# Optimization experiments

Hardware: AMD Instinct MI355X
Metric: run time of the kernel (lower is better)

Reference implementation:

```python
import jax, jax.numpy as jnp
import numpy as np

K = 7          # kernel_size
GC = 16        # group_channels (hardcoded in module)
EPS = 1e-5     # BatchNorm eps


def setup_inputs() -> dict:
    key = jax.random.key(0)
    ks = jax.random.split(key, 4)
    B, C, H, W = 4, 256, 56, 56
    Cr = C // 4                      # reduction_ratio = 4
    G = C // GC                      # groups = 16
    return {
        "x": jax.random.normal(ks[0], (B, C, H, W), jnp.float32),
        "conv1_w": jax.random.normal(ks[1], (Cr, C), jnp.float32) * 0.05,
        "bn_gamma": jnp.ones((Cr,), jnp.float32),
        "bn_beta": jnp.zeros((Cr,), jnp.float32),
        "bn_mean": jnp.zeros((Cr,), jnp.float32),
        "bn_var": jnp.ones((Cr,), jnp.float32),
        "conv2_w": jax.random.normal(ks[2], (K * K * G, Cr), jnp.float32) * 0.05,
        "conv2_b": jax.random.normal(ks[3], (K * K * G,), jnp.float32) * 0.05,
    }


def _unfold(x, k):
    # torch nn.Unfold with padding=(k-1)//2, stride=1 -> [B, C, k*k, H, W]
    B, C, H, W = x.shape
    p = (k - 1) // 2
    xp = jnp.pad(x, ((0, 0), (0, 0), (p, p), (p, p)))
    patches = jnp.stack(
        [xp[:, :, i:i + H, j:j + W] for i in range(k) for j in range(k)],
        axis=2,
    )  # (kh, kw) flattened, channel-slowest -> matches torch unfold layout
    return patches


def reference(x, conv1_w, bn_gamma, bn_beta, bn_mean, bn_var, conv2_w, conv2_b):
    B, C, H, W = x.shape
    G = C // GC
    # kernel-generation branch (stride == 1, no avgpool)
    w = jnp.einsum('bchw,oc->bohw', x, conv1_w)                 # conv1 1x1
    inv_std = jax.lax.rsqrt(bn_var + EPS)
    w = (w - bn_mean[None, :, None, None]) * (bn_gamma * inv_std)[None, :, None, None] \
        + bn_beta[None, :, None, None]                           # BN (eval)
    w = jax.nn.relu(w)
    w = jnp.einsum('bchw,oc->bohw', w, conv2_w) + conv2_b[None, :, None, None]
    w = w.reshape(B, G, K * K, H, W)                             # [B,G,K2,H,W]
    # unfold + weighted reduce
    patches = _unfold(x, K).reshape(B, G, GC, K * K, H, W)       # [B,G,gc,K2,H,W]
    out = jnp.einsum('bgkhw,bgckhw->bgchw', w, patches)          # sum over K2
    return out.reshape(B, C, H, W)
```

## Files before the change

kernel.cpp:

```cpp
#include <hip/hip_runtime.h>


#define EPS 1e-5f

typedef __fp16 half2t __attribute__((ext_vector_type(2)));
typedef __fp16 half8t __attribute__((ext_vector_type(8)));
typedef float floatx4 __attribute__((ext_vector_type(4)));

__device__ inline half8t pack8(float4 u0, float4 u1, float s) {
    half8t a;
    half2t q;
    q = __builtin_amdgcn_cvt_pkrtz(u0.x * s, u0.y * s); a[0] = q[0]; a[1] = q[1];
    q = __builtin_amdgcn_cvt_pkrtz(u0.z * s, u0.w * s); a[2] = q[0]; a[3] = q[1];
    q = __builtin_amdgcn_cvt_pkrtz(u1.x * s, u1.y * s); a[4] = q[0]; a[5] = q[1];
    q = __builtin_amdgcn_cvt_pkrtz(u1.z * s, u1.w * s); a[6] = q[0]; a[7] = q[1];
    return a;
}

__global__ __launch_bounds__(256, 4) void k1_conv1(
    const float* __restrict__ x, const float* __restrict__ w1,
    const float* __restrict__ gamma, const float* __restrict__ beta,
    const float* __restrict__ mean, const float* __restrict__ var,
    __fp16* __restrict__ mid)
{
    __shared__ __align__(16) __fp16 lxB[32 * 72];
    const int t    = threadIdx.x;
    const int b    = blockIdx.y;
    const int p0   = blockIdx.x * 32;
    const int lane = t & 63, wvid = t >> 6;
    const int mrow = lane & 15, quad = lane >> 4;

    const int orow = wvid * 16 + mrow;
    const float s = gamma[orow] * rsqrtf(var[orow] + EPS);
    half8t A[4][2];
#pragma unroll
    for (int ch = 0; ch < 4; ++ch)
#pragma unroll
        for (int h = 0; h < 2; ++h) {
            const float* src = &w1[orow * 256 + ch * 64 + h * 32 + quad * 8];
            A[ch][h] = pack8(*(const float4*)src, *(const float4*)(src + 4), s);
        }

    floatx4 acc[2] = {};
    const int c2 = t & 31, pxq = t >> 5;
    for (int ch = 0; ch < 4; ++ch) {
        const float* r0 = &x[(size_t)(b * 256 + ch * 64 + 2 * c2) * 3136 + p0 + pxq * 4];
        const float* r1 = r0 + 3136;
        float4 a0 = *(const float4*)r0;
        float4 b0 = *(const float4*)r1;
        const float* f0 = (const float*)&a0;
        const float* f1 = (const float*)&b0;
#pragma unroll
        for (int j = 0; j < 4; ++j) {
            half2t q = __builtin_amdgcn_cvt_pkrtz(f0[j], f1[j]);
            *(half2t*)&lxB[(pxq * 4 + j) * 72 + 2 * c2] = q;
        }
        __syncthreads();
#pragma unroll
        for (int pt = 0; pt < 2; ++pt) {
            half8t bf0 = *(const half8t*)&lxB[(pt * 16 + mrow) * 72 + quad * 8];
            half8t bf1 = *(const half8t*)&lxB[(pt * 16 + mrow) * 72 + quad * 8 + 32];
            acc[pt] = __builtin_amdgcn_mfma_f32_16x16x32_f16(A[ch][0], bf0, acc[pt], 0, 0, 0);
            acc[pt] = __builtin_amdgcn_mfma_f32_16x16x32_f16(A[ch][1], bf1, acc[pt], 0, 0, 0);
        }
        __syncthreads();
    }
    float bb[4];
#pragma unroll
    for (int i = 0; i < 4; ++i) {
        int o = wvid * 16 + quad * 4 + i;
        float so = gamma[o] * rsqrtf(var[o] + EPS);
        bb[i] = beta[o] - mean[o] * so;
    }
#pragma unroll
    for (int pt = 0; pt < 2; ++pt)
#pragma unroll
        for (int i = 0; i < 4; ++i) {
            float v = fmaxf(acc[pt][i] + bb[i], 0.f);
            lxB[(pt * 16 + mrow) * 72 + wvid * 16 + quad * 4 + i] = (__fp16)v;
        }
    __syncthreads();
    {
        int px = t >> 3, o8 = t & 7;
        *(half8t*)&mid[(size_t)(b * 3136 + p0 + px) * 64 + o8 * 8] =
            *(const half8t*)&lxB[px * 72 + o8 * 8];
    }
}

__global__ __launch_bounds__(256, 5) void k23_fused(
    const float* __restrict__ x, const __fp16* __restrict__ mid,
    const float* __restrict__ cw, const float* __restrict__ cb,
    float* __restrict__ out)
{
    __shared__ __align__(16) unsigned char smem[28944];
    __fp16* lmid = (__fp16*)smem;
    float*  lx   = (float*)smem;
    float*  lw2  = (float*)(smem + 15616);

    const int t  = threadIdx.x;
    const int b  = blockIdx.z;
    const int g  = blockIdx.y;
    const int th = blockIdx.x / 7, tw = blockIdx.x % 7;
    const int h0 = th * 8, w0 = tw * 8;
    const int lane = t & 63, wvid = t >> 6;
    const int mrow = lane & 15, quad = lane >> 4;

    float4 rv4[4];
    int    rslot[4];
#pragma unroll
    for (int i = 0; i < 4; ++i) {
        int s = t + i * 256;
        rslot[i] = s;
        float4 v = make_float4(0.f, 0.f, 0.f, 0.f);
        if (s < 896) {
            int ch = s / 56, r = s % 56;
            int row = r >> 2, q = r & 3;
            int gh = h0 + row - 3;
            int gwb = w0 - 4 + q * 4;
            bool ok = (gh >= 0) & (gh < 56) & (gwb >= 0) & (gwb <= 52);
            int ghc = min(max(gh, 0), 55);
            int gwc = min(max(gwb, 0), 52);
            float4 ld = *(const float4*)&x[(size_t)(b * 256 + g * 16 + ch) * 3136 +
                                           ghc * 56 + gwc];
            if (ok) v = ld;
        }
        rv4[i] = v;
    }

    const int krow = wvid * 16 + mrow;
    half8t a0 = {}, a1 = {};
    if (krow < 49) {
        const float* src = &cw[(size_t)(g * 49 + krow) * 64 + quad * 8];
        a0 = pack8(*(const float4*)src,        *(const float4*)(src + 4),  1.f);
        a1 = pack8(*(const float4*)(src + 32), *(const float4*)(src + 36), 1.f);
    }

#pragma unroll
    for (int i = 0; i < 2; ++i) {
        int s  = t + i * 256;
        int px = s >> 3, c8 = s & 7;
        int pix = (h0 + (px >> 3)) * 56 + w0 + (px & 7);
        *(half8t*)&lmid[px * 72 + c8 * 8] =
            *(const half8t*)&mid[(size_t)(b * 3136 + pix) * 64 + c8 * 8];
    }
    __syncthreads();

    {
        float bias[4];
        int   kor[4];
#pragma unroll
        for (int i = 0; i < 4; ++i) {
            kor[i]  = wvid * 16 + quad * 4 + i;
            bias[i] = (kor[i] < 49) ? cb[g * 49 + kor[i]] : 0.f;
        }
#pragma unroll
        for (int pt = 0; pt < 4; ++pt) {
            half8t b0 = *(const half8t*)&lmid[(pt * 16 + mrow) * 72 + quad * 8];
            half8t b1 = *(const half8t*)&lmid[(pt * 16 + mrow) * 72 + quad * 8 + 32];
            floatx4 acc = {0.f, 0.f, 0.f, 0.f};
            acc = __builtin_amdgcn_mfma_f32_16x16x32_f16(a0, b0, acc, 0, 0, 0);
            acc = __builtin_amdgcn_mfma_f32_16x16x32_f16(a1, b1, acc, 0, 0, 0);
#pragma unroll
            for (int i = 0; i < 4; ++i)
                if (kor[i] < 49)
                    lw2[kor[i] * 68 + pt * 16 + mrow] = acc[i] + bias[i];
        }
    }
    __syncthreads();

#pragma unroll
    for (int i = 0; i < 4; ++i) {
        int s = rslot[i];
        if (s < 896) {
            int ch = s / 56, r = s % 56;
            int row = r >> 2, q = r & 3;
            float* dst = &lx[ch * 244 + row * 17 + q * 4];
            dst[0] = rv4[i].x; dst[1] = rv4[i].y;
            dst[2] = rv4[i].z; dst[3] = rv4[i].w;
        }
    }
    __syncthreads();

    const int cc = t >> 4, pxt = t & 15;
    const int sh = pxt >> 1, sw4 = (pxt & 1) * 4;
    float a0f = 0.f, a1f = 0.f, a2f = 0.f, a3f = 0.f;
#pragma unroll
    for (int kh = 0; kh < 7; ++kh) {
        float xr[10];
        const int base = cc * 244 + (sh + kh) * 17 + sw4 + 1;
#pragma unroll
        for (int j = 0; j < 10; ++j) xr[j] = lx[base + j];
#pragma unroll
        for (int kw = 0; kw < 7; ++kw) {
            const float4 wv = *(const float4*)&lw2[(kh * 7 + kw) * 68 + pxt * 4];
            a0f = fmaf(wv.x, xr[kw + 0], a0f);
            a1f = fmaf(wv.y, xr[kw + 1], a1f);
            a2f = fmaf(wv.z, xr[kw + 2], a2f);
            a3f = fmaf(wv.w, xr[kw + 3], a3f);
        }
    }
    *(float4*)&out[(b * 256 + g * 16 + cc) * 3136 + (h0 + sh) * 56 + w0 + sw4] =
        make_float4(a0f, a1f, a2f, a3f);
}

extern "C" void kernel_launch(void* const* d_in, const int* in_sizes, int n_in,
                              void* d_out, int out_size, void* d_ws, size_t ws_size,
                              hipStream_t stream) {
    const float* x     = (const float*)d_in[0];
    const float* w1    = (const float*)d_in[1];
    const float* gamma = (const float*)d_in[2];
    const float* beta  = (const float*)d_in[3];
    const float* mean  = (const float*)d_in[4];
    const float* var   = (const float*)d_in[5];
    const float* cw    = (const float*)d_in[6];
    const float* cb    = (const float*)d_in[7];
    float* out = (float*)d_out;

    __fp16* mid = (__fp16*)d_ws;

    k1_conv1<<<dim3(98, 4), 256, 0, stream>>>(x, w1, gamma, beta, mean, var, mid);
    k23_fused<<<dim3(49, 16, 4), 256, 0, stream>>>(x, mid, cw, cb, out);
}
```

Measured before the change: 106.8 us.

## Process two groups per block with fp16 staging and register-blocked unfold

Restructures the fused kernel so each 128-thread block handles two groups, one wave per group. Each wave computes all 49 dynamic kernel rows for its group with MFMA, reusing the shared mid tile across both groups. The x halo tile and the generated weights are now stored in LDS as fp16 instead of fp32, roughly halving LDS footprint and traffic. The inner unfold loop is register-blocked over 4 channels × 4 pixels so each loaded weight vector is reused across several channels. The risks are extra fp16 rounding in x and the weights, a higher register load (14 half4 prefetch registers plus a 16-float accumulator), and fewer threads per block.

```diff
diff --git a/kernel.cpp b/kernel.cpp
--- a/kernel.cpp
+++ b/kernel.cpp
@@ -4,6 +4,7 @@
 #define EPS 1e-5f
 
 typedef __fp16 half2t __attribute__((ext_vector_type(2)));
+typedef __fp16 half4t __attribute__((ext_vector_type(4)));
 typedef __fp16 half8t __attribute__((ext_vector_type(8)));
 typedef float floatx4 __attribute__((ext_vector_type(4)));
 
@@ -87,57 +88,48 @@
     }
 }
 
-__global__ __launch_bounds__(256, 5) void k23_fused(
+__global__ __launch_bounds__(128, 3) void k2_fused(
     const float* __restrict__ x, const __fp16* __restrict__ mid,
     const float* __restrict__ cw, const float* __restrict__ cb,
     float* __restrict__ out)
 {
-    __shared__ __align__(16) unsigned char smem[28944];
+    __shared__ __align__(16) unsigned char smem[28960];
     __fp16* lmid = (__fp16*)smem;
-    float*  lx   = (float*)smem;
-    float*  lw2  = (float*)(smem + 15616);
+    __fp16* lxh  = (__fp16*)smem;
 
     const int t  = threadIdx.x;
     const int b  = blockIdx.z;
-    const int g  = blockIdx.y;
+    const int gq = blockIdx.y;
     const int th = blockIdx.x / 7, tw = blockIdx.x % 7;
     const int h0 = th * 8, w0 = tw * 8;
     const int lane = t & 63, wvid = t >> 6;
     const int mrow = lane & 15, quad = lane >> 4;
-
-    float4 rv4[4];
-    int    rslot[4];
+    const int g = gq * 2 + wvid;
+    __fp16* lw2h = (__fp16*)(smem + 14848 + wvid * 7056);
+
+    half4t hr[14];
+#pragma unroll
+    for (int i = 0; i < 14; ++i) {
+        int s = t + i * 128;
+        int ch = s / 56, r = s % 56;
+        int row = r >> 2, cq = r & 3;
+        int gh = h0 + row - 3;
+        int gwb = w0 - 4 + cq * 4;
+        bool ok = (gh >= 0) & (gh < 56) & (gwb >= 0) & (gwb <= 52);
+        int ghc = min(max(gh, 0), 55);
+        int gwc = min(max(gwb, 0), 52);
+        float4 ld = *(const float4*)&x[(size_t)(b * 256 + gq * 32 + ch) * 3136 +
+                                       ghc * 56 + gwc];
+        if (!ok) ld = make_float4(0.f, 0.f, 0.f, 0.f);
+        half2t p0 = __builtin_amdgcn_cvt_pkrtz(ld.x, ld.y);
+        half2t p1 = __builtin_amdgcn_cvt_pkrtz(ld.z, ld.w);
+        half4t h; h[0] = p0[0]; h[1] = p0[1]; h[2] = p1[0]; h[3] = p1[1];
+        hr[i] = h;
+    }
+
 #pragma unroll
     for (int i = 0; i < 4; ++i) {
-        int s = t + i * 256;
-        rslot[i] = s;
-        float4 v = make_float4(0.f, 0.f, 0.f, 0.f);
-        if (s < 896) {
-            int ch = s / 56, r = s % 56;
-            int row = r >> 2, q = r & 3;
-            int gh = h0 + row - 3;
-            int gwb = w0 - 4 + q * 4;
-            bool ok = (gh >= 0) & (gh < 56) & (gwb >= 0) & (gwb <= 52);
-            int ghc = min(max(gh, 0), 55);
-            int gwc = min(max(gwb, 0), 52);
-            float4 ld = *(const float4*)&x[(size_t)(b * 256 + g * 16 + ch) * 3136 +
-                                           ghc * 56 + gwc];
-            if (ok) v = ld;
-        }
-        rv4[i] = v;
-    }
-
-    const int krow = wvid * 16 + mrow;
-    half8t a0 = {}, a1 = {};
-    if (krow < 49) {
-        const float* src = &cw[(size_t)(g * 49 + krow) * 64 + quad * 8];
-        a0 = pack8(*(const float4*)src,        *(const float4*)(src + 4),  1.f);
-        a1 = pack8(*(const float4*)(src + 32), *(const float4*)(src + 36), 1.f);
-    }
-
-#pragma unroll
-    for (int i = 0; i < 2; ++i) {
-        int s  = t + i * 256;
+        int s  = t + i * 128;
         int px = s >> 3, c8 = s & 7;
         int pix = (h0 + (px >> 3)) * 56 + w0 + (px & 7);
         *(half8t*)&lmid[px * 72 + c8 * 8] =
@@ -146,61 +138,80 @@
     __syncthreads();
 
     {
-        float bias[4];
-        int   kor[4];
-#pragma unroll
-        for (int i = 0; i < 4; ++i) {
-            kor[i]  = wvid * 16 + quad * 4 + i;
-            bias[i] = (kor[i] < 49) ? cb[g * 49 + kor[i]] : 0.f;
-        }
+        half8t bf[4][2];
 #pragma unroll
         for (int pt = 0; pt < 4; ++pt) {
-            half8t b0 = *(const half8t*)&lmid[(pt * 16 + mrow) * 72 + quad * 8];
-            half8t b1 = *(const half8t*)&lmid[(pt * 16 + mrow) * 72 + quad * 8 + 32];
-            floatx4 acc = {0.f, 0.f, 0.f, 0.f};
-            acc = __builtin_amdgcn_mfma_f32_16x16x32_f16(a0, b0, acc, 0, 0, 0);
-            acc = __builtin_amdgcn_mfma_f32_16x16x32_f16(a1, b1, acc, 0, 0, 0);
-#pragma unroll
-            for (int i = 0; i < 4; ++i)
-                if (kor[i] < 49)
-                    lw2[kor[i] * 68 + pt * 16 + mrow] = acc[i] + bias[i];
-        }
-    }
-    __syncthreads();
-
+            bf[pt][0] = *(const half8t*)&lmid[(pt * 16 + mrow) * 72 + quad * 8];
+            bf[pt][1] = *(const half8t*)&lmid[(pt * 16 + mrow) * 72 + quad * 8 + 32];
+        }
+#pragma unroll
+        for (int mc = 0; mc < 4; ++mc) {
+            int krow = mc * 16 + mrow;
+            half8t a0 = {}, a1 = {};
+            if (krow < 49) {
+                const float* src = &cw[(size_t)(g * 49 + krow) * 64 + quad * 8];
+                a0 = pack8(*(const float4*)src,        *(const float4*)(src + 4),  1.f);
+                a1 = pack8(*(const float4*)(src + 32), *(const float4*)(src + 36), 1.f);
+            }
+#pragma unroll
+            for (int pt = 0; pt < 4; ++pt) {
+                floatx4 acc = {0.f, 0.f, 0.f, 0.f};
+                acc = __builtin_amdgcn_mfma_f32_16x16x32_f16(a0, bf[pt][0], acc, 0, 0, 0);
+                acc = __builtin_amdgcn_mfma_f32_16x16x32_f16(a1, bf[pt][1], acc, 0, 0, 0);
+                int px = pt * 16 + mrow;
+#pragma unroll
+                for (int i = 0; i < 4; ++i) {
+                    int ko = mc * 16 + quad * 4 + i;
+                    if (ko < 49)
+                        lw2h[ko * 72 + px] = (__fp16)(acc[i] + cb[g * 49 + ko]);
+                }
+            }
+        }
+    }
+    __syncthreads();
+
+#pragma unroll
+    for (int i = 0; i < 14; ++i) {
+        int s = t + i * 128;
+        int ch = s / 56, r = s % 56;
+        int row = r >> 2, cq = r & 3;
+        *(half4t*)&lxh[ch * 232 + row * 16 + cq * 4] = hr[i];
+    }
+    __syncthreads();
+
+    const int cc  = lane >> 4;
+    const int pxt = lane & 15;
+    const int sh  = pxt >> 1, sw4 = (pxt & 1) * 4;
+    const int chb = wvid * 16 + cc * 4;
+    float acc[4][4] = {};
+#pragma unroll
+    for (int kh = 0; kh < 7; ++kh) {
+        const int row = sh + kh;
+        half4t xq[4][3];
+#pragma unroll
+        for (int i = 0; i < 4; ++i)
+#pragma unroll
+            for (int q = 0; q < 3; ++q)
+                xq[i][q] = *(const half4t*)&lxh[(chb + i) * 232 + row * 16 + sw4 + q * 4];
+#pragma unroll
+        for (int kw = 0; kw < 7; ++kw) {
+            half4t wq = *(const half4t*)&lw2h[(kh * 7 + kw) * 72 + pxt * 4];
+#pragma unroll
+            for (int j = 0; j < 4; ++j) {
+                const int o = 1 + kw + j;
+#pragma unroll
+                for (int i = 0; i < 4; ++i)
+                    acc[i][j] = fmaf((float)wq[j], (float)xq[i][o >> 2][o & 3],
+                                     acc[i][j]);
+            }
+        }
+    }
 #pragma unroll
     for (int i = 0; i < 4; ++i) {
-        int s = rslot[i];
-        if (s < 896) {
-            int ch = s / 56, r = s % 56;
-            int row = r >> 2, q = r & 3;
-            float* dst = &lx[ch * 244 + row * 17 + q * 4];
-            dst[0] = rv4[i].x; dst[1] = rv4[i].y;
-            dst[2] = rv4[i].z; dst[3] = rv4[i].w;
-        }
-    }
-    __syncthreads();
-
-    const int cc = t >> 4, pxt = t & 15;
-    const int sh = pxt >> 1, sw4 = (pxt & 1) * 4;
-    float a0f = 0.f, a1f = 0.f, a2f = 0.f, a3f = 0.f;
-#pragma unroll
-    for (int kh = 0; kh < 7; ++kh) {
-        float xr[10];
-        const int base = cc * 244 + (sh + kh) * 17 + sw4 + 1;
-#pragma unroll
-        for (int j = 0; j < 10; ++j) xr[j] = lx[base + j];
-#pragma unroll
-        for (int kw = 0; kw < 7; ++kw) {
-            const float4 wv = *(const float4*)&lw2[(kh * 7 + kw) * 68 + pxt * 4];
-            a0f = fmaf(wv.x, xr[kw + 0], a0f);
-            a1f = fmaf(wv.y, xr[kw + 1], a1f);
-            a2f = fmaf(wv.z, xr[kw + 2], a2f);
-            a3f = fmaf(wv.w, xr[kw + 3], a3f);
-        }
-    }
-    *(float4*)&out[(b * 256 + g * 16 + cc) * 3136 + (h0 + sh) * 56 + w0 + sw4] =
-        make_float4(a0f, a1f, a2f, a3f);
+        *(float4*)&out[(size_t)(b * 256 + g * 16 + cc * 4 + i) * 3136 +
+                       (h0 + sh) * 56 + w0 + sw4] =
+            make_float4(acc[i][0], acc[i][1], acc[i][2], acc[i][3]);
+    }
 }
 
 extern "C" void kernel_launch(void* const* d_in, const int* in_sizes, int n_in,
@@ -219,5 +230,5 @@
     __fp16* mid = (__fp16*)d_ws;
 
     k1_conv1<<<dim3(98, 4), 256, 0, stream>>>(x, w1, gamma, beta, mean, var, mid);
-    k23_fused<<<dim3(49, 16, 4), 256, 0, stream>>>(x, mid, cw, cb, out);
-}
+    k2_fused<<<dim3(49, 8, 4), 128, 0, stream>>>(x, mid, cw, cb, out);
+}
```

New measurement: 124.5 us. +16.6%, slower.

## Fuse conv1+BN+ReLU into the involution kernel, recomputing per group block

Applied to the files above, without the earlier changes.

Removes the separate conv1 kernel and its fp16 intermediate buffer by computing the 1x1 conv, BN and ReLU for each 8x8 tile inside the fused involution kernel. This eliminates one launch and the global write/read of the mid tensor. In exchange, every one of the 16 group blocks for a tile recomputes the full conv1 and rereads all 256 input channels, multiplying that work and traffic. Shared memory also grows, which may reduce occupancy.

```diff
diff --git a/kernel.cpp b/kernel.cpp
--- a/kernel.cpp
+++ b/kernel.cpp
@@ -17,85 +17,18 @@
     return a;
 }
 
-__global__ __launch_bounds__(256, 4) void k1_conv1(
+__global__ __launch_bounds__(256, 4) void k_fused(
     const float* __restrict__ x, const float* __restrict__ w1,
     const float* __restrict__ gamma, const float* __restrict__ beta,
     const float* __restrict__ mean, const float* __restrict__ var,
-    __fp16* __restrict__ mid)
-{
-    __shared__ __align__(16) __fp16 lxB[32 * 72];
-    const int t    = threadIdx.x;
-    const int b    = blockIdx.y;
-    const int p0   = blockIdx.x * 32;
-    const int lane = t & 63, wvid = t >> 6;
-    const int mrow = lane & 15, quad = lane >> 4;
-
-    const int orow = wvid * 16 + mrow;
-    const float s = gamma[orow] * rsqrtf(var[orow] + EPS);
-    half8t A[4][2];
-#pragma unroll
-    for (int ch = 0; ch < 4; ++ch)
-#pragma unroll
-        for (int h = 0; h < 2; ++h) {
-            const float* src = &w1[orow * 256 + ch * 64 + h * 32 + quad * 8];
-            A[ch][h] = pack8(*(const float4*)src, *(const float4*)(src + 4), s);
-        }
-
-    floatx4 acc[2] = {};
-    const int c2 = t & 31, pxq = t >> 5;
-    for (int ch = 0; ch < 4; ++ch) {
-        const float* r0 = &x[(size_t)(b * 256 + ch * 64 + 2 * c2) * 3136 + p0 + pxq * 4];
-        const float* r1 = r0 + 3136;
-        float4 a0 = *(const float4*)r0;
-        float4 b0 = *(const float4*)r1;
-        const float* f0 = (const float*)&a0;
-        const float* f1 = (const float*)&b0;
-#pragma unroll
-        for (int j = 0; j < 4; ++j) {
-            half2t q = __builtin_amdgcn_cvt_pkrtz(f0[j], f1[j]);
-            *(half2t*)&lxB[(pxq * 4 + j) * 72 + 2 * c2] = q;
-        }
-        __syncthreads();
-#pragma unroll
-        for (int pt = 0; pt < 2; ++pt) {
-            half8t bf0 = *(const half8t*)&lxB[(pt * 16 + mrow) * 72 + quad * 8];
-            half8t bf1 = *(const half8t*)&lxB[(pt * 16 + mrow) * 72 + quad * 8 + 32];
-            acc[pt] = __builtin_amdgcn_mfma_f32_16x16x32_f16(A[ch][0], bf0, acc[pt], 0, 0, 0);
-            acc[pt] = __builtin_amdgcn_mfma_f32_16x16x32_f16(A[ch][1], bf1, acc[pt], 0, 0, 0);
-        }
-        __syncthreads();
-    }
-    float bb[4];
-#pragma unroll
-    for (int i = 0; i < 4; ++i) {
-        int o = wvid * 16 + quad * 4 + i;
-        float so = gamma[o] * rsqrtf(var[o] + EPS);
-        bb[i] = beta[o] - mean[o] * so;
-    }
-#pragma unroll
-    for (int pt = 0; pt < 2; ++pt)
-#pragma unroll
-        for (int i = 0; i < 4; ++i) {
-            float v = fmaxf(acc[pt][i] + bb[i], 0.f);
-            lxB[(pt * 16 + mrow) * 72 + wvid * 16 + quad * 4 + i] = (__fp16)v;
-        }
-    __syncthreads();
-    {
-        int px = t >> 3, o8 = t & 7;
-        *(half8t*)&mid[(size_t)(b * 3136 + p0 + px) * 64 + o8 * 8] =
-            *(const half8t*)&lxB[px * 72 + o8 * 8];
-    }
-}
-
-__global__ __launch_bounds__(256, 5) void k23_fused(
-    const float* __restrict__ x, const __fp16* __restrict__ mid,
     const float* __restrict__ cw, const float* __restrict__ cb,
     float* __restrict__ out)
 {
-    __shared__ __align__(16) unsigned char smem[28944];
-    __fp16* lmid = (__fp16*)smem;
+    __shared__ __align__(16) unsigned char smem[31760];
+    __fp16* bufA = (__fp16*)smem;
+    __fp16* lmid = (__fp16*)(smem + 9216);
     float*  lx   = (float*)smem;
-    float*  lw2  = (float*)(smem + 15616);
+    float*  lw2  = (float*)(smem + 18432);
 
     const int t  = threadIdx.x;
     const int b  = blockIdx.z;
@@ -105,22 +38,58 @@
     const int lane = t & 63, wvid = t >> 6;
     const int mrow = lane & 15, quad = lane >> 4;
 
+    const int orow = wvid * 16 + mrow;
+    const float s1 = gamma[orow] * rsqrtf(var[orow] + EPS);
+
+    const int c2 = t & 31, px8 = t >> 5;
+    floatx4 acc1[4] = {};
+#pragma unroll
+    for (int ch = 0; ch < 4; ++ch) {
+        const float* r0 = &x[(size_t)(b * 256 + ch * 64 + 2 * c2) * 3136 +
+                             (h0 + px8) * 56 + w0];
+        float4 xa0 = *(const float4*)r0;
+        float4 xa1 = *(const float4*)(r0 + 4);
+        float4 xb0 = *(const float4*)(r0 + 3136);
+        float4 xb1 = *(const float4*)(r0 + 3140);
+        const float* wsrc = &w1[orow * 256 + ch * 64 + quad * 8];
+        half8t A0 = pack8(*(const float4*)wsrc,        *(const float4*)(wsrc + 4),  s1);
+        half8t A1 = pack8(*(const float4*)(wsrc + 32), *(const float4*)(wsrc + 36), s1);
+
+        float fa[8], fb[8];
+        fa[0]=xa0.x; fa[1]=xa0.y; fa[2]=xa0.z; fa[3]=xa0.w;
+        fa[4]=xa1.x; fa[5]=xa1.y; fa[6]=xa1.z; fa[7]=xa1.w;
+        fb[0]=xb0.x; fb[1]=xb0.y; fb[2]=xb0.z; fb[3]=xb0.w;
+        fb[4]=xb1.x; fb[5]=xb1.y; fb[6]=xb1.z; fb[7]=xb1.w;
+#pragma unroll
+        for (int j = 0; j < 8; ++j) {
+            half2t q = __builtin_amdgcn_cvt_pkrtz(fa[j], fb[j]);
+            *(half2t*)&bufA[(px8 * 8 + j) * 72 + 2 * c2] = q;
+        }
+        __syncthreads();
+#pragma unroll
+        for (int pt = 0; pt < 4; ++pt) {
+            half8t bf0 = *(const half8t*)&bufA[(pt * 16 + mrow) * 72 + quad * 8];
+            half8t bf1 = *(const half8t*)&bufA[(pt * 16 + mrow) * 72 + quad * 8 + 32];
+            acc1[pt] = __builtin_amdgcn_mfma_f32_16x16x32_f16(A0, bf0, acc1[pt], 0, 0, 0);
+            acc1[pt] = __builtin_amdgcn_mfma_f32_16x16x32_f16(A1, bf1, acc1[pt], 0, 0, 0);
+        }
+        __syncthreads();
+    }
+
     float4 rv4[4];
-    int    rslot[4];
 #pragma unroll
     for (int i = 0; i < 4; ++i) {
         int s = t + i * 256;
-        rslot[i] = s;
         float4 v = make_float4(0.f, 0.f, 0.f, 0.f);
         if (s < 896) {
-            int ch = s / 56, r = s % 56;
+            int chh = s / 56, r = s % 56;
             int row = r >> 2, q = r & 3;
             int gh = h0 + row - 3;
             int gwb = w0 - 4 + q * 4;
             bool ok = (gh >= 0) & (gh < 56) & (gwb >= 0) & (gwb <= 52);
             int ghc = min(max(gh, 0), 55);
             int gwc = min(max(gwb, 0), 52);
-            float4 ld = *(const float4*)&x[(size_t)(b * 256 + g * 16 + ch) * 3136 +
+            float4 ld = *(const float4*)&x[(size_t)(b * 256 + g * 16 + chh) * 3136 +
                                            ghc * 56 + gwc];
             if (ok) v = ld;
         }
@@ -135,13 +104,21 @@
         a1 = pack8(*(const float4*)(src + 32), *(const float4*)(src + 36), 1.f);
     }
 
-#pragma unroll
-    for (int i = 0; i < 2; ++i) {
-        int s  = t + i * 256;
-        int px = s >> 3, c8 = s & 7;
-        int pix = (h0 + (px >> 3)) * 56 + w0 + (px & 7);
-        *(half8t*)&lmid[px * 72 + c8 * 8] =
-            *(const half8t*)&mid[(size_t)(b * 3136 + pix) * 64 + c8 * 8];
+    {
+        float bb[4];
+#pragma unroll
+        for (int i = 0; i < 4; ++i) {
+            int o = wvid * 16 + quad * 4 + i;
+            float so = gamma[o] * rsqrtf(var[o] + EPS);
+            bb[i] = beta[o] - mean[o] * so;
+        }
+#pragma unroll
+        for (int pt = 0; pt < 4; ++pt)
+#pragma unroll
+            for (int i = 0; i < 4; ++i) {
+                float v = fmaxf(acc1[pt][i] + bb[i], 0.f);
+                lmid[(pt * 16 + mrow) * 72 + wvid * 16 + quad * 4 + i] = (__fp16)v;
+            }
     }
     __syncthreads();
 
@@ -170,11 +147,11 @@
 
 #pragma unroll
     for (int i = 0; i < 4; ++i) {
-        int s = rslot[i];
+        int s = t + i * 256;
         if (s < 896) {
-            int ch = s / 56, r = s % 56;
+            int chh = s / 56, r = s % 56;
             int row = r >> 2, q = r & 3;
-            float* dst = &lx[ch * 244 + row * 17 + q * 4];
+            float* dst = &lx[chh * 244 + row * 17 + q * 4];
             dst[0] = rv4[i].x; dst[1] = rv4[i].y;
             dst[2] = rv4[i].z; dst[3] = rv4[i].w;
         }
@@ -216,8 +193,8 @@
     const float* cb    = (const float*)d_in[7];
     float* out = (float*)d_out;
 
-    __fp16* mid = (__fp16*)d_ws;
-
-    k1_conv1<<<dim3(98, 4), 256, 0, stream>>>(x, w1, gamma, beta, mean, var, mid);
-    k23_fused<<<dim3(49, 16, 4), 256, 0, stream>>>(x, mid, cw, cb, out);
+    (void)d_ws; (void)ws_size;
+
+    k_fused<<<dim3(49, 16, 4), 256, 0, stream>>>(x, w1, gamma, beta, mean, var,
+                                                 cw, cb, out);
 }
```

Measured after the change: 145.4 us. 1.36x slower.
